# Kernel optimization log

Hardware: AMD Instinct MI355X
Metric: run time of the kernel (lower is better)

## Reference

```python
import jax, jax.numpy as jnp
import numpy as np


def _ln(x, w, b):
    m = x.mean(-1, keepdims=True)
    v = ((x - m) ** 2).mean(-1, keepdims=True)
    return (x - m) / jnp.sqrt(v + 1e-5) * w + b


def setup_inputs() -> dict:
    key = jax.random.key(0)
    ks = jax.random.split(key, 8)
    N, C, H, W = 2, 64, 128, 128
    heads, ksz = 2, 7
    C4 = 4 * C
    p = lambda k, shape: jax.random.normal(k, shape, dtype=jnp.float32) * 0.02
    return {
        "x": jax.random.normal(ks[0], (N, C, H, W), dtype=jnp.float32),
        "qkv_w": p(ks[1], (3 * C, C)),
        "qkv_b": jnp.zeros((3 * C,), jnp.float32),
        "proj_w": p(ks[2], (C, C)),
        "proj_b": jnp.zeros((C,), jnp.float32),
        "rpb": p(ks[3], (heads, 2 * ksz - 1, 2 * ksz - 1)),
        "ln1_w": jnp.ones((C,), jnp.float32),
        "ln1_b": jnp.zeros((C,), jnp.float32),
        "ln2_w": jnp.ones((C,), jnp.float32),
        "ln2_b": jnp.zeros((C,), jnp.float32),
        "fc1_w": p(ks[4], (C4, C)),
        "fc1_b": jnp.zeros((C4,), jnp.float32),
        "fc2_w": p(ks[5], (C, C4)),
        "fc2_b": jnp.zeros((C,), jnp.float32),
    }


def reference(x, qkv_w, qkv_b, proj_w, proj_b, rpb, ln1_w, ln1_b, ln2_w, ln2_b,
              fc1_w, fc1_b, fc2_w, fc2_b):
    N, C, H, W = x.shape
    heads = rpb.shape[0]
    ksz = (rpb.shape[1] + 1) // 2  # kernel size from (2k-1) bias table
    dh = C // heads

    xt = x.transpose(0, 2, 3, 1).reshape(N, H * W, C)  # n (h w) c
    shortcut = xt
    xn = _ln(xt, ln1_w, ln1_b).reshape(N, H, W, C)

    # qkv projection -> (3, N, heads, H, W, dh)
    qkv = (xn @ qkv_w.T + qkv_b).reshape(N, H, W, 3, heads, dh)
    qkv = qkv.transpose(3, 0, 4, 1, 2, 5)
    q = qkv[0] * (dh ** -0.5)
    k = qkv[1]
    v = qkv[2]

    # NATTEN neighborhood: window start clamped so every query sees k x k keys
    sh = jnp.clip(jnp.arange(H) - ksz // 2, 0, H - ksz)
    sw = jnp.clip(jnp.arange(W) - ksz // 2, 0, W - ksz)
    rows = sh[:, None] + jnp.arange(ksz)  # (H, k) key row indices
    cols = sw[:, None] + jnp.arange(ksz)  # (W, k) key col indices

    # relative position bias index: (query - key) + (k-1) in [0, 2k-2]
    rel_h = jnp.arange(H)[:, None] - rows + (ksz - 1)  # (H, k)
    rel_w = jnp.arange(W)[:, None] - cols + (ksz - 1)  # (W, k)
    bias = rpb[:, rel_h][:, :, :, rel_w]               # (heads, H, k, W, k)
    bias = bias.transpose(0, 1, 3, 2, 4)               # (heads, H, W, k, k)

    ri = rows[:, None, :, None]  # (H,1,k,1)
    ci = cols[None, :, None, :]  # (1,W,1,k)
    kwin = k[:, :, ri, ci, :]    # (N, heads, H, W, k, k, dh)
    vwin = v[:, :, ri, ci, :]

    scores = jnp.einsum('nzhwd,nzhwijd->nzhwij', q, kwin) + bias[None]
    attn = jax.nn.softmax(scores.reshape(N, heads, H, W, ksz * ksz), axis=-1)
    out = jnp.einsum('nzhwe,nzhwed->nzhwd', attn,
                     vwin.reshape(N, heads, H, W, ksz * ksz, dh))
    out = out.transpose(0, 2, 3, 1, 4).reshape(N, H, W, C) @ proj_w.T + proj_b

    x2 = shortcut + out.reshape(N, H * W, C)
    y = _ln(x2, ln2_w, ln2_b)
    y = jax.nn.gelu(y @ fc1_w.T + fc1_b, approximate=False) @ fc2_w.T + fc2_b
    x3 = x2 + y
    return x3.reshape(N, H, W, C).transpose(0, 3, 1, 2)
```

## Files before the change

### kernel.cpp

```cpp
#include <hip/hip_runtime.h>
#include <math.h>

#define TQ   32768
#define HWSZ 16384
#define CC   64
#define HH   128
#define WW   128
#define C3   192
#define C4   256
#define KS   7

typedef _Float16 half2v __attribute__((ext_vector_type(2)));
typedef _Float16 half4v __attribute__((ext_vector_type(4)));
typedef _Float16 half8v __attribute__((ext_vector_type(8)));
typedef float    f32x4  __attribute__((ext_vector_type(4)));

#define MFMA16(a, b, c) __builtin_amdgcn_mfma_f32_16x16x32_f16((a), (b), (c), 0, 0, 0)

__global__ __launch_bounds__(256) void k_qkvln(const float* __restrict__ x,
        const float* __restrict__ lnw, const float* __restrict__ lnb,
        const float* __restrict__ qw, const float* __restrict__ qb,
        _Float16* __restrict__ qkv16) {
    __shared__ union {
        struct { __align__(16) _Float16 A[128 * 72]; __align__(16) _Float16 B[192 * 72]; } st;
        __align__(16) _Float16 outb[128 * 200];
    } u;
    __shared__ float ps1[256], ps2[256], m_s[128], r_s[128];
    __shared__ float w_s[64], b_s[64], bias_s[192];
    int tid = threadIdx.x;
    int t0 = blockIdx.x * 128;
    if (tid < 64) { w_s[tid] = lnw[tid]; b_s[tid] = lnb[tid]; }
    if (tid < 192) bias_s[tid] = qb[tid];
    int tok = tid & 127, cq = tid >> 7;
    int t = t0 + tok;
    int n = t >> 14, hw = t & (HWSZ - 1);
    const float* xr = x + ((size_t)n << 20) + hw;
    float v[32];
    float s = 0.f, s2 = 0.f;
#pragma unroll
    for (int e = 0; e < 32; ++e) {
        float f = xr[(cq * 32 + e) * HWSZ];
        v[e] = f; s += f; s2 += f * f;
    }
    ps1[tid] = s; ps2[tid] = s2;
    for (int i = tid; i < 3072; i += 256) {
        int jj = i >> 4, seg = i & 15;
        float4 v4 = *(const float4*)&qw[(size_t)jj * 64 + seg * 4];
        half4v h4 = { (_Float16)v4.x, (_Float16)v4.y, (_Float16)v4.z, (_Float16)v4.w };
        *(half4v*)&u.st.B[jj * 72 + seg * 4] = h4;
    }
    __syncthreads();
    if (tid < 128) {
        float ss = ps1[tid] + ps1[tid + 128];
        float qq = ps2[tid] + ps2[tid + 128];
        float m = ss * (1.f / 64.f);
        float var = qq * (1.f / 64.f) - m * m;
        m_s[tid] = m; r_s[tid] = rsqrtf(var + 1e-5f);
    }
    __syncthreads();
    {
        float m = m_s[tok], r = r_s[tok];
#pragma unroll
        for (int u8 = 0; u8 < 4; ++u8) {
            half8v o;
#pragma unroll
            for (int e = 0; e < 8; ++e) {
                int c = cq * 32 + u8 * 8 + e;
                o[e] = (_Float16)((v[u8 * 8 + e] - m) * r * w_s[c] + b_s[c]);
            }
            *(half8v*)&u.st.A[tok * 72 + cq * 32 + u8 * 8] = o;
        }
    }
    __syncthreads();
    int lane = tid & 63, wv = tid >> 6;
    int quad = lane >> 4, l16 = lane & 15;
    int mt0 = (wv & 1) * 64, nt0 = (wv >> 1) * 96;
    f32x4 acc[4][6];
#pragma unroll
    for (int mf = 0; mf < 4; ++mf)
#pragma unroll
        for (int nf = 0; nf < 6; ++nf) acc[mf][nf] = (f32x4){0.f, 0.f, 0.f, 0.f};
#pragma unroll
    for (int ks = 0; ks < 64; ks += 32) {
        half8v a[4], bfr[6];
#pragma unroll
        for (int mf = 0; mf < 4; ++mf)
            a[mf] = *(const half8v*)&u.st.A[(mt0 + mf * 16 + l16) * 72 + ks + quad * 8];
#pragma unroll
        for (int nf = 0; nf < 6; ++nf)
            bfr[nf] = *(const half8v*)&u.st.B[(nt0 + nf * 16 + l16) * 72 + ks + quad * 8];
#pragma unroll
        for (int mf = 0; mf < 4; ++mf)
#pragma unroll
            for (int nf = 0; nf < 6; ++nf) acc[mf][nf] = MFMA16(a[mf], bfr[nf], acc[mf][nf]);
    }
    __syncthreads();
    const float qscale = 0.17677669529663687f;
#pragma unroll
    for (int mf = 0; mf < 4; ++mf)
#pragma unroll
        for (int nf = 0; nf < 6; ++nf) {
            int j = nt0 + nf * 16 + l16;
            float bias = bias_s[j];
            float sc = (j < 64) ? qscale : 1.f;
#pragma unroll
            for (int r = 0; r < 4; ++r) {
                int tl = mt0 + mf * 16 + quad * 4 + r;
                u.outb[tl * 200 + j] = (_Float16)((acc[mf][nf][r] + bias) * sc);
            }
        }
    __syncthreads();
    for (int i = tid; i < 4096; i += 256) {
        int tk = i >> 5, rem = i & 31;
        if (rem < 24)
            *(half8v*)&qkv16[(size_t)(t0 + tk) * C3 + rem * 8] =
                *(const half8v*)&u.outb[tk * 200 + rem * 8];
    }
}

#define KV_STRIDE 136
#define QS_STRIDE 80
#define SS_STRIDE 50

__global__ __launch_bounds__(256) void k_attn(const _Float16* __restrict__ qkv16,
        const float* __restrict__ rpb, _Float16* __restrict__ out) {
    __shared__ __align__(16) _Float16 kv_s[196 * KV_STRIDE];
    __shared__ __align__(16) _Float16 q_s[64 * QS_STRIDE];
    __shared__ __align__(16) _Float16 s_s[128 * SS_STRIDE];
    __shared__ float rpb_s[338];

    int tid = threadIdx.x;
    int bx = blockIdx.x;
    int n  = bx >> 8;
    int th = (bx >> 4) & 15, tw = bx & 15;
    int h0 = th * 8, w0 = tw * 8;
    int wr0 = min(max(h0 - 3, 0), HH - 14);
    int ww0 = min(max(w0 - 3, 0), WW - 14);
    int tbase = n << 14;

    for (int i = tid; i < 338; i += 256) rpb_s[i] = rpb[i];
    for (int i = tid; i < 196 * 16; i += 256) {
        int tok = i >> 4, u = i & 15;
        int wi = tok / 14, wj = tok - wi * 14;
        *(half8v*)&kv_s[tok * KV_STRIDE + u * 8] = *(const half8v*)&qkv16[
            (size_t)(tbase + (wr0 + wi) * WW + ww0 + wj) * C3 + 64 + u * 8];
    }
    for (int i = tid; i < 64 * 8; i += 256) {
        int q = i >> 3, u = i & 7;
        int qg = tbase + (h0 + (q >> 3)) * WW + (w0 + (q & 7));
        *(half8v*)&q_s[q * QS_STRIDE + u * 8] = *(const half8v*)&qkv16[(size_t)qg * C3 + u * 8];
    }
    __syncthreads();

    int half_ = tid & 1, z = (tid >> 1) & 1, q = tid >> 2;
    int qy = q >> 3, qx = q & 7;
    int h = h0 + qy, wc = w0 + qx;
    int sh = min(max(h - 3, 0), HH - KS);
    int sw = min(max(wc - 3, 0), WW - KS);
    int oh = sh - wr0, ow = sw - ww0;
    int dhp = h - sh + 6, dwp = wc - sw + 6;
    {
        const half8v* qp = (const half8v*)&q_s[q * QS_STRIDE + z * 32];
        half8v q0 = qp[0], q1 = qp[1], q2 = qp[2], q3 = qp[3];
        int i7 = 0, j7 = half_;
        for (int nb = half_; nb < 49; nb += 2) {
            int tok = (oh + i7) * 14 + (ow + j7);
            const half8v* kp = (const half8v*)&kv_s[tok * KV_STRIDE + z * 32];
            half2v acc2 = { (_Float16)0.f, (_Float16)0.f };
            half8v k0 = kp[0], k1 = kp[1], k2 = kp[2], k3 = kp[3];
            acc2 += (half2v){k0.s0, k0.s1} * (half2v){q0.s0, q0.s1};
            acc2 += (half2v){k0.s2, k0.s3} * (half2v){q0.s2, q0.s3};
            acc2 += (half2v){k0.s4, k0.s5} * (half2v){q0.s4, q0.s5};
            acc2 += (half2v){k0.s6, k0.s7} * (half2v){q0.s6, q0.s7};
            acc2 += (half2v){k1.s0, k1.s1} * (half2v){q1.s0, q1.s1};
            acc2 += (half2v){k1.s2, k1.s3} * (half2v){q1.s2, q1.s3};
            acc2 += (half2v){k1.s4, k1.s5} * (half2v){q1.s4, q1.s5};
            acc2 += (half2v){k1.s6, k1.s7} * (half2v){q1.s6, q1.s7};
            acc2 += (half2v){k2.s0, k2.s1} * (half2v){q2.s0, q2.s1};
            acc2 += (half2v){k2.s2, k2.s3} * (half2v){q2.s2, q2.s3};
            acc2 += (half2v){k2.s4, k2.s5} * (half2v){q2.s4, q2.s5};
            acc2 += (half2v){k2.s6, k2.s7} * (half2v){q2.s6, q2.s7};
            acc2 += (half2v){k3.s0, k3.s1} * (half2v){q3.s0, q3.s1};
            acc2 += (half2v){k3.s2, k3.s3} * (half2v){q3.s2, q3.s3};
            acc2 += (half2v){k3.s4, k3.s5} * (half2v){q3.s4, q3.s5};
            acc2 += (half2v){k3.s6, k3.s7} * (half2v){q3.s6, q3.s7};
            float s = (float)acc2.x + (float)acc2.y
                    + rpb_s[(z * 13 + (dhp - i7)) * 13 + (dwp - j7)];
            s_s[(q * 2 + z) * SS_STRIDE + nb] = (_Float16)s;
            j7 += 2;
            if (j7 >= 7) { j7 -= 7; ++i7; }
        }
    }
    __syncthreads();

    if (tid < 128) {
        _Float16* sp = &s_s[tid * SS_STRIDE];
        float mx = -1e30f;
        for (int i = 0; i < 49; ++i) mx = fmaxf(mx, (float)sp[i]);
        float sum = 0.f;
        for (int i = 0; i < 49; ++i) {
            float e = __expf((float)sp[i] - mx);
            sum += e;
            sp[i] = (_Float16)e;
        }
        float inv = 1.f / sum;
        for (int i = 0; i < 49; ++i) sp[i] = (_Float16)((float)sp[i] * inv);
    }
    __syncthreads();

    {
        int c16 = half_;
        const _Float16* pp = &s_s[(q * 2 + z) * SS_STRIDE];
        half2v acc[8];
#pragma unroll
        for (int j = 0; j < 8; ++j) acc[j] = (half2v){ (_Float16)0.f, (_Float16)0.f };
        int i7 = 0, j7 = 0;
        for (int nb = 0; nb < 49; ++nb) {
            int tok = (oh + i7) * 14 + (ow + j7);
            _Float16 p = pp[nb];
            half2v p2 = { p, p };
            const half8v* vp = (const half8v*)&kv_s[tok * KV_STRIDE + 64 + z * 32 + c16 * 16];
            half8v v0 = vp[0], v1 = vp[1];
            acc[0] += (half2v){v0.s0, v0.s1} * p2;
            acc[1] += (half2v){v0.s2, v0.s3} * p2;
            acc[2] += (half2v){v0.s4, v0.s5} * p2;
            acc[3] += (half2v){v0.s6, v0.s7} * p2;
            acc[4] += (half2v){v1.s0, v1.s1} * p2;
            acc[5] += (half2v){v1.s2, v1.s3} * p2;
            acc[6] += (half2v){v1.s4, v1.s5} * p2;
            acc[7] += (half2v){v1.s6, v1.s7} * p2;
            ++j7;
            if (j7 == 7) { j7 = 0; ++i7; }
        }
        int qg = tbase + h * WW + wc;
        _Float16* op = out + (size_t)qg * CC + z * 32 + c16 * 16;
        half8v o0 = {acc[0].x, acc[0].y, acc[1].x, acc[1].y, acc[2].x, acc[2].y, acc[3].x, acc[3].y};
        half8v o1 = {acc[4].x, acc[4].y, acc[5].x, acc[5].y, acc[6].x, acc[6].y, acc[7].x, acc[7].y};
        *(half8v*)op = o0;
        *(half8v*)(op + 8) = o1;
    }
}

__global__ __launch_bounds__(256) void k_projln(const _Float16* __restrict__ ain,
        const float* __restrict__ pw, const float* __restrict__ pb,
        const float* __restrict__ x,
        const float* __restrict__ ln2w, const float* __restrict__ ln2b,
        _Float16* __restrict__ x2_16, _Float16* __restrict__ xn2_16) {
    __shared__ union {
        struct { __align__(16) _Float16 A[128 * 72]; __align__(16) _Float16 B[64 * 72]; } st;
        float x2t[128 * 67];
    } u;
    __shared__ float ps1[256], ps2[256], m_s[128], r_s[128];
    __shared__ float w_s[64], b_s[64], pbias[64];
    int tid = threadIdx.x;
    int t0 = blockIdx.x * 128;
    int n = t0 >> 14, hw0 = t0 & (HWSZ - 1);
    if (tid < 64) { w_s[tid] = ln2w[tid]; b_s[tid] = ln2b[tid]; pbias[tid] = pb[tid]; }
    for (int i = tid; i < 1024; i += 256) {
        int tok = i >> 3, u8 = i & 7;
        *(half8v*)&u.st.A[tok * 72 + u8 * 8] = *(const half8v*)&ain[(size_t)(t0 + tok) * 64 + u8 * 8];
    }
    for (int i = tid; i < 1024; i += 256) {
        int jj = i >> 4, seg = i & 15;
        float4 v4 = *(const float4*)&pw[(size_t)jj * 64 + seg * 4];
        half4v h4 = { (_Float16)v4.x, (_Float16)v4.y, (_Float16)v4.z, (_Float16)v4.w };
        *(half4v*)&u.st.B[jj * 72 + seg * 4] = h4;
    }
    __syncthreads();
    int lane = tid & 63, wv = tid >> 6;
    int quad = lane >> 4, l16 = lane & 15;
    int mt0 = wv * 32;
    f32x4 acc[2][4];
#pragma unroll
    for (int mf = 0; mf < 2; ++mf)
#pragma unroll
        for (int nf = 0; nf < 4; ++nf) acc[mf][nf] = (f32x4){0.f, 0.f, 0.f, 0.f};
#pragma unroll
    for (int ks = 0; ks < 64; ks += 32) {
        half8v a[2], bfr[4];
#pragma unroll
        for (int mf = 0; mf < 2; ++mf)
            a[mf] = *(const half8v*)&u.st.A[(mt0 + mf * 16 + l16) * 72 + ks + quad * 8];
#pragma unroll
        for (int nf = 0; nf < 4; ++nf)
            bfr[nf] = *(const half8v*)&u.st.B[(nf * 16 + l16) * 72 + ks + quad * 8];
#pragma unroll
        for (int mf = 0; mf < 2; ++mf)
#pragma unroll
            for (int nf = 0; nf < 4; ++nf) acc[mf][nf] = MFMA16(a[mf], bfr[nf], acc[mf][nf]);
    }
    __syncthreads();
#pragma unroll
    for (int mf = 0; mf < 2; ++mf)
#pragma unroll
        for (int nf = 0; nf < 4; ++nf) {
            int j = nf * 16 + l16;
            float bias = pbias[j];
            int hwl = hw0 + mt0 + mf * 16 + quad * 4;
            float4 rx = *(const float4*)&x[((size_t)(n * CC + j) << 14) + hwl];
#pragma unroll
            for (int r = 0; r < 4; ++r) {
                int tl = mt0 + mf * 16 + quad * 4 + r;
                u.x2t[tl * 67 + j] = acc[mf][nf][r] + bias + ((const float*)&rx)[r];
            }
        }
    __syncthreads();
    int tok = tid & 127, cq = tid >> 7;
    {
        float s = 0.f, s2 = 0.f;
#pragma unroll
        for (int e = 0; e < 32; ++e) {
            float f = u.x2t[tok * 67 + cq * 32 + e];
            s += f; s2 += f * f;
        }
        ps1[tid] = s; ps2[tid] = s2;
    }
    __syncthreads();
    if (tid < 128) {
        float ss = ps1[tid] + ps1[tid + 128];
        float qq = ps2[tid] + ps2[tid + 128];
        float m = ss * (1.f / 64.f);
        float var = qq * (1.f / 64.f) - m * m;
        m_s[tid] = m; r_s[tid] = rsqrtf(var + 1e-5f);
    }
    __syncthreads();
    {
        float m = m_s[tok], r = r_s[tok];
#pragma unroll
        for (int u8 = 0; u8 < 4; ++u8) {
            half8v hv, nv;
#pragma unroll
            for (int e = 0; e < 8; ++e) {
                int c = cq * 32 + u8 * 8 + e;
                float f = u.x2t[tok * 67 + c];
                hv[e] = (_Float16)f;
                nv[e] = (_Float16)((f - m) * r * w_s[c] + b_s[c]);
            }
            size_t base = (size_t)(t0 + tok) * 64 + cq * 32 + u8 * 8;
            *(half8v*)&x2_16[base] = hv;
            *(half8v*)&xn2_16[base] = nv;
        }
    }
}

__global__ __launch_bounds__(256) void k_fc1(const _Float16* __restrict__ xin,
        const float* __restrict__ fw, const float* __restrict__ fb,
        _Float16* __restrict__ hbuf16) {
    __shared__ __align__(16) _Float16 A_s[128 * 72];
    __shared__ __align__(16) _Float16 B_s[128 * 72];
    __shared__ float bias_s[128];
    int tid = threadIdx.x;
    int t0 = (blockIdx.x >> 1) * 128;
    int j0 = (blockIdx.x & 1) * 128;
    for (int i = tid; i < 1024; i += 256) {
        int tok = i >> 3, u8 = i & 7;
        *(half8v*)&A_s[tok * 72 + u8 * 8] = *(const half8v*)&xin[(size_t)(t0 + tok) * 64 + u8 * 8];
    }
    for (int i = tid; i < 2048; i += 256) {
        int jj = i >> 4, seg = i & 15;
        float4 v4 = *(const float4*)&fw[(size_t)(j0 + jj) * 64 + seg * 4];
        half4v h4 = { (_Float16)v4.x, (_Float16)v4.y, (_Float16)v4.z, (_Float16)v4.w };
        *(half4v*)&B_s[jj * 72 + seg * 4] = h4;
    }
    if (tid < 128) bias_s[tid] = fb[j0 + tid];
    __syncthreads();
    int lane = tid & 63, wv = tid >> 6;
    int quad = lane >> 4, l16 = lane & 15;
    int mt0 = (wv & 1) * 64, nt0 = (wv >> 1) * 64;
    f32x4 acc[4][4];
#pragma unroll
    for (int mf = 0; mf < 4; ++mf)
#pragma unroll
        for (int nf = 0; nf < 4; ++nf) acc[mf][nf] = (f32x4){0.f, 0.f, 0.f, 0.f};
#pragma unroll
    for (int ks = 0; ks < 64; ks += 32) {
        half8v a[4], bfr[4];
#pragma unroll
        for (int mf = 0; mf < 4; ++mf)
            a[mf] = *(const half8v*)&A_s[(mt0 + mf * 16 + l16) * 72 + ks + quad * 8];
#pragma unroll
        for (int nf = 0; nf < 4; ++nf)
            bfr[nf] = *(const half8v*)&B_s[(nt0 + nf * 16 + l16) * 72 + ks + quad * 8];
#pragma unroll
        for (int mf = 0; mf < 4; ++mf)
#pragma unroll
            for (int nf = 0; nf < 4; ++nf) acc[mf][nf] = MFMA16(a[mf], bfr[nf], acc[mf][nf]);
    }
#pragma unroll
    for (int mf = 0; mf < 4; ++mf)
#pragma unroll
        for (int nf = 0; nf < 4; ++nf) {
            int j = j0 + nt0 + nf * 16 + l16;
            float bias = bias_s[nt0 + nf * 16 + l16];
#pragma unroll
            for (int r = 0; r < 4; ++r) {
                int t = t0 + mt0 + mf * 16 + quad * 4 + r;
                float v = acc[mf][nf][r] + bias;
                float g = 0.5f * v * (1.f + erff(v * 0.70710678118654752f));
                hbuf16[(size_t)t * C4 + j] = (_Float16)g;
            }
        }
}

__global__ __launch_bounds__(256) void k_fc2(const _Float16* __restrict__ hbuf16,
        const float* __restrict__ fw, const float* __restrict__ fb,
        const _Float16* __restrict__ x2_16, float* __restrict__ out) {
    __shared__ union {
        struct { __align__(16) _Float16 A[128 * 72]; __align__(16) _Float16 B[64 * 72]; } st;
        float tr[64 * 132];
    } u;
    __shared__ float fb_s[64];
    int tid = threadIdx.x;
    int t0 = blockIdx.x * 128;
    int lane = tid & 63, wv = tid >> 6;
    int quad = lane >> 4, l16 = lane & 15;
    int mt0 = wv * 32;
    if (tid < 64) fb_s[tid] = fb[tid];
    f32x4 acc[2][4];
#pragma unroll
    for (int mf = 0; mf < 2; ++mf)
#pragma unroll
        for (int nf = 0; nf < 4; ++nf) acc[mf][nf] = (f32x4){0.f, 0.f, 0.f, 0.f};
    for (int kp = 0; kp < 4; ++kp) {
        if (kp) __syncthreads();
        for (int i = tid; i < 1024; i += 256) {
            int tok = i >> 3, u8 = i & 7;
            *(half8v*)&u.st.A[tok * 72 + u8 * 8] =
                *(const half8v*)&hbuf16[(size_t)(t0 + tok) * C4 + kp * 64 + u8 * 8];
        }
        for (int i = tid; i < 1024; i += 256) {
            int jj = i >> 4, seg = i & 15;
            float4 v4 = *(const float4*)&fw[(size_t)jj * C4 + kp * 64 + seg * 4];
            half4v h4 = { (_Float16)v4.x, (_Float16)v4.y, (_Float16)v4.z, (_Float16)v4.w };
            *(half4v*)&u.st.B[jj * 72 + seg * 4] = h4;
        }
        __syncthreads();
#pragma unroll
        for (int ks = 0; ks < 64; ks += 32) {
            half8v a[2], bfr[4];
#pragma unroll
            for (int mf = 0; mf < 2; ++mf)
                a[mf] = *(const half8v*)&u.st.A[(mt0 + mf * 16 + l16) * 72 + ks + quad * 8];
#pragma unroll
            for (int nf = 0; nf < 4; ++nf)
                bfr[nf] = *(const half8v*)&u.st.B[(nf * 16 + l16) * 72 + ks + quad * 8];
#pragma unroll
            for (int mf = 0; mf < 2; ++mf)
#pragma unroll
                for (int nf = 0; nf < 4; ++nf) acc[mf][nf] = MFMA16(a[mf], bfr[nf], acc[mf][nf]);
        }
    }
    __syncthreads();
#pragma unroll
    for (int mf = 0; mf < 2; ++mf)
#pragma unroll
        for (int nf = 0; nf < 4; ++nf) {
            int j = nf * 16 + l16;
            float bias = fb_s[j];
#pragma unroll
            for (int r = 0; r < 4; ++r) {
                int tl = mt0 + mf * 16 + quad * 4 + r;
                float v = acc[mf][nf][r] + bias + (float)x2_16[(size_t)(t0 + tl) * 64 + j];
                u.tr[j * 132 + tl] = v;
            }
        }
    __syncthreads();
    int n = t0 >> 14, hw0 = t0 & (HWSZ - 1);
    for (int i = tid; i < 64 * 32; i += 256) {
        int j = i >> 5, seg = i & 31;
        float4 v = *(const float4*)&u.tr[j * 132 + seg * 4];
        *(float4*)&out[((size_t)(n * CC + j) << 14) + hw0 + seg * 4] = v;
    }
}

extern "C" void kernel_launch(void* const* d_in, const int* in_sizes, int n_in,
                              void* d_out, int out_size, void* d_ws, size_t ws_size,
                              hipStream_t stream) {
    const float* x      = (const float*)d_in[0];
    const float* qkv_w  = (const float*)d_in[1];
    const float* qkv_b  = (const float*)d_in[2];
    const float* proj_w = (const float*)d_in[3];
    const float* proj_b = (const float*)d_in[4];
    const float* rpb    = (const float*)d_in[5];
    const float* ln1_w  = (const float*)d_in[6];
    const float* ln1_b  = (const float*)d_in[7];
    const float* ln2_w  = (const float*)d_in[8];
    const float* ln2_b  = (const float*)d_in[9];
    const float* fc1_w  = (const float*)d_in[10];
    const float* fc1_b  = (const float*)d_in[11];
    const float* fc2_w  = (const float*)d_in[12];
    const float* fc2_b  = (const float*)d_in[13];
    float* out = (float*)d_out;
    char* ws = (char*)d_ws;

    _Float16* qkv16  = (_Float16*)(ws);
    _Float16* attn16 = (_Float16*)(ws + 12582912);
    _Float16* x2_16  = (_Float16*)(ws + 16777216);
    _Float16* xn2_16 = (_Float16*)(ws + 20971520);
    _Float16* hbuf16 = (_Float16*)(ws + 25165824);

    k_qkvln <<<256, 256, 0, stream>>>(x, ln1_w, ln1_b, qkv_w, qkv_b, qkv16);
    k_attn  <<<512, 256, 0, stream>>>(qkv16, rpb, attn16);
    k_projln<<<256, 256, 0, stream>>>(attn16, proj_w, proj_b, x, ln2_w, ln2_b, x2_16, xn2_16);
    k_fc1   <<<512, 256, 0, stream>>>(xn2_16, fc1_w, fc1_b, hbuf16);
    k_fc2   <<<256, 256, 0, stream>>>(hbuf16, fc2_w, fc2_b, x2_16, out);
}
```

Baseline: 149.6 us.

## Fuse fc1 and fc2 into one MLP kernel keeping hidden activations in LDS

```diff
diff --git a/kernel.cpp b/kernel.cpp
--- a/kernel.cpp
+++ b/kernel.cpp
@@ -343,132 +343,113 @@
     }
 }
 
-__global__ __launch_bounds__(256) void k_fc1(const _Float16* __restrict__ xin,
-        const float* __restrict__ fw, const float* __restrict__ fb,
-        _Float16* __restrict__ hbuf16) {
-    __shared__ __align__(16) _Float16 A_s[128 * 72];
-    __shared__ __align__(16) _Float16 B_s[128 * 72];
-    __shared__ float bias_s[128];
+__global__ __launch_bounds__(256) void k_mlp(const _Float16* __restrict__ xn2,
+        const _Float16* __restrict__ x2_16,
+        const float* __restrict__ f1w, const float* __restrict__ f1b,
+        const float* __restrict__ f2w, const float* __restrict__ f2b,
+        float* __restrict__ out) {
+    __shared__ __align__(16) _Float16 H_s[64 * 264];
+    __shared__ union {
+        struct { __align__(16) _Float16 A[64 * 72]; __align__(16) _Float16 B[128 * 72]; } st;
+        float tr[64 * 68];
+    } u;
+    __shared__ float f1b_s[256], f2b_s[64];
     int tid = threadIdx.x;
-    int t0 = (blockIdx.x >> 1) * 128;
-    int j0 = (blockIdx.x & 1) * 128;
-    for (int i = tid; i < 1024; i += 256) {
-        int tok = i >> 3, u8 = i & 7;
-        *(half8v*)&A_s[tok * 72 + u8 * 8] = *(const half8v*)&xin[(size_t)(t0 + tok) * 64 + u8 * 8];
-    }
-    for (int i = tid; i < 2048; i += 256) {
-        int jj = i >> 4, seg = i & 15;
-        float4 v4 = *(const float4*)&fw[(size_t)(j0 + jj) * 64 + seg * 4];
-        half4v h4 = { (_Float16)v4.x, (_Float16)v4.y, (_Float16)v4.z, (_Float16)v4.w };
-        *(half4v*)&B_s[jj * 72 + seg * 4] = h4;
-    }
-    if (tid < 128) bias_s[tid] = fb[j0 + tid];
-    __syncthreads();
+    int t0 = blockIdx.x * 64;
     int lane = tid & 63, wv = tid >> 6;
     int quad = lane >> 4, l16 = lane & 15;
-    int mt0 = (wv & 1) * 64, nt0 = (wv >> 1) * 64;
-    f32x4 acc[4][4];
-#pragma unroll
-    for (int mf = 0; mf < 4; ++mf)
-#pragma unroll
-        for (int nf = 0; nf < 4; ++nf) acc[mf][nf] = (f32x4){0.f, 0.f, 0.f, 0.f};
-#pragma unroll
-    for (int ks = 0; ks < 64; ks += 32) {
-        half8v a[4], bfr[4];
-#pragma unroll
-        for (int mf = 0; mf < 4; ++mf)
-            a[mf] = *(const half8v*)&A_s[(mt0 + mf * 16 + l16) * 72 + ks + quad * 8];
-#pragma unroll
-        for (int nf = 0; nf < 4; ++nf)
-            bfr[nf] = *(const half8v*)&B_s[(nt0 + nf * 16 + l16) * 72 + ks + quad * 8];
-#pragma unroll
-        for (int mf = 0; mf < 4; ++mf)
-#pragma unroll
-            for (int nf = 0; nf < 4; ++nf) acc[mf][nf] = MFMA16(a[mf], bfr[nf], acc[mf][nf]);
-    }
-#pragma unroll
-    for (int mf = 0; mf < 4; ++mf)
-#pragma unroll
-        for (int nf = 0; nf < 4; ++nf) {
-            int j = j0 + nt0 + nf * 16 + l16;
-            float bias = bias_s[nt0 + nf * 16 + l16];
-#pragma unroll
-            for (int r = 0; r < 4; ++r) {
-                int t = t0 + mt0 + mf * 16 + quad * 4 + r;
-                float v = acc[mf][nf][r] + bias;
-                float g = 0.5f * v * (1.f + erff(v * 0.70710678118654752f));
-                hbuf16[(size_t)t * C4 + j] = (_Float16)g;
+    f1b_s[tid] = f1b[tid];
+    if (tid < 64) f2b_s[tid] = f2b[tid];
+    for (int i = tid; i < 512; i += 256) {
+        int tok = i >> 3, u8 = i & 7;
+        *(half8v*)&u.st.A[tok * 72 + u8 * 8] = *(const half8v*)&xn2[(size_t)(t0 + tok) * 64 + u8 * 8];
+    }
+    for (int jh = 0; jh < 2; ++jh) {
+        if (jh) __syncthreads();
+        for (int i = tid; i < 2048; i += 256) {
+            int jj = i >> 4, seg = i & 15;
+            float4 v4 = *(const float4*)&f1w[(size_t)(jh * 128 + jj) * 64 + seg * 4];
+            half4v h4 = { (_Float16)v4.x, (_Float16)v4.y, (_Float16)v4.z, (_Float16)v4.w };
+            *(half4v*)&u.st.B[jj * 72 + seg * 4] = h4;
+        }
+        __syncthreads();
+        int mt0 = (wv & 1) * 32, nt0 = (wv >> 1) * 64;
+        f32x4 acc[2][4];
+#pragma unroll
+        for (int mf = 0; mf < 2; ++mf)
+#pragma unroll
+            for (int nf = 0; nf < 4; ++nf) acc[mf][nf] = (f32x4){0.f, 0.f, 0.f, 0.f};
+#pragma unroll
+        for (int ks = 0; ks < 64; ks += 32) {
+            half8v a[2], bfr[4];
+#pragma unroll
+            for (int mf = 0; mf < 2; ++mf)
+                a[mf] = *(const half8v*)&u.st.A[(mt0 + mf * 16 + l16) * 72 + ks + quad * 8];
+#pragma unroll
+            for (int nf = 0; nf < 4; ++nf)
+                bfr[nf] = *(const half8v*)&u.st.B[(nt0 + nf * 16 + l16) * 72 + ks + quad * 8];
+#pragma unroll
+            for (int mf = 0; mf < 2; ++mf)
+#pragma unroll
+                for (int nf = 0; nf < 4; ++nf) acc[mf][nf] = MFMA16(a[mf], bfr[nf], acc[mf][nf]);
+        }
+#pragma unroll
+        for (int mf = 0; mf < 2; ++mf)
+#pragma unroll
+            for (int nf = 0; nf < 4; ++nf) {
+                int jl = nt0 + nf * 16 + l16;
+                float bias = f1b_s[jh * 128 + jl];
+#pragma unroll
+                for (int r = 0; r < 4; ++r) {
+                    int tl = mt0 + mf * 16 + quad * 4 + r;
+                    float vv = acc[mf][nf][r] + bias;
+                    float g = 0.5f * vv * (1.f + erff(vv * 0.70710678118654752f));
+                    H_s[tl * 264 + jh * 128 + jl] = (_Float16)g;
+                }
             }
-        }
-}
-
-__global__ __launch_bounds__(256) void k_fc2(const _Float16* __restrict__ hbuf16,
-        const float* __restrict__ fw, const float* __restrict__ fb,
-        const _Float16* __restrict__ x2_16, float* __restrict__ out) {
-    __shared__ union {
-        struct { __align__(16) _Float16 A[128 * 72]; __align__(16) _Float16 B[64 * 72]; } st;
-        float tr[64 * 132];
-    } u;
-    __shared__ float fb_s[64];
-    int tid = threadIdx.x;
-    int t0 = blockIdx.x * 128;
-    int lane = tid & 63, wv = tid >> 6;
-    int quad = lane >> 4, l16 = lane & 15;
-    int mt0 = wv * 32;
-    if (tid < 64) fb_s[tid] = fb[tid];
-    f32x4 acc[2][4];
-#pragma unroll
-    for (int mf = 0; mf < 2; ++mf)
-#pragma unroll
-        for (int nf = 0; nf < 4; ++nf) acc[mf][nf] = (f32x4){0.f, 0.f, 0.f, 0.f};
+    }
+    __syncthreads();
+    int mt0 = wv * 16;
+    f32x4 acc2[4];
+#pragma unroll
+    for (int nf = 0; nf < 4; ++nf) acc2[nf] = (f32x4){0.f, 0.f, 0.f, 0.f};
     for (int kp = 0; kp < 4; ++kp) {
         if (kp) __syncthreads();
         for (int i = tid; i < 1024; i += 256) {
-            int tok = i >> 3, u8 = i & 7;
-            *(half8v*)&u.st.A[tok * 72 + u8 * 8] =
-                *(const half8v*)&hbuf16[(size_t)(t0 + tok) * C4 + kp * 64 + u8 * 8];
-        }
-        for (int i = tid; i < 1024; i += 256) {
             int jj = i >> 4, seg = i & 15;
-            float4 v4 = *(const float4*)&fw[(size_t)jj * C4 + kp * 64 + seg * 4];
+            float4 v4 = *(const float4*)&f2w[(size_t)jj * C4 + kp * 64 + seg * 4];
             half4v h4 = { (_Float16)v4.x, (_Float16)v4.y, (_Float16)v4.z, (_Float16)v4.w };
             *(half4v*)&u.st.B[jj * 72 + seg * 4] = h4;
         }
         __syncthreads();
 #pragma unroll
         for (int ks = 0; ks < 64; ks += 32) {
-            half8v a[2], bfr[4];
-#pragma unroll
-            for (int mf = 0; mf < 2; ++mf)
-                a[mf] = *(const half8v*)&u.st.A[(mt0 + mf * 16 + l16) * 72 + ks + quad * 8];
+            half8v a = *(const half8v*)&H_s[(mt0 + l16) * 264 + kp * 64 + ks + quad * 8];
+            half8v bfr[4];
 #pragma unroll
             for (int nf = 0; nf < 4; ++nf)
                 bfr[nf] = *(const half8v*)&u.st.B[(nf * 16 + l16) * 72 + ks + quad * 8];
 #pragma unroll
-            for (int mf = 0; mf < 2; ++mf)
-#pragma unroll
-                for (int nf = 0; nf < 4; ++nf) acc[mf][nf] = MFMA16(a[mf], bfr[nf], acc[mf][nf]);
-        }
-    }
-    __syncthreads();
-#pragma unroll
-    for (int mf = 0; mf < 2; ++mf)
-#pragma unroll
-        for (int nf = 0; nf < 4; ++nf) {
-            int j = nf * 16 + l16;
-            float bias = fb_s[j];
-#pragma unroll
-            for (int r = 0; r < 4; ++r) {
-                int tl = mt0 + mf * 16 + quad * 4 + r;
-                float v = acc[mf][nf][r] + bias + (float)x2_16[(size_t)(t0 + tl) * 64 + j];
-                u.tr[j * 132 + tl] = v;
-            }
-        }
+            for (int nf = 0; nf < 4; ++nf) acc2[nf] = MFMA16(a, bfr[nf], acc2[nf]);
+        }
+    }
+    __syncthreads();
+#pragma unroll
+    for (int nf = 0; nf < 4; ++nf) {
+        int j = nf * 16 + l16;
+        float bias = f2b_s[j];
+#pragma unroll
+        for (int r = 0; r < 4; ++r) {
+            int tl = mt0 + quad * 4 + r;
+            float v = acc2[nf][r] + bias + (float)x2_16[(size_t)(t0 + tl) * 64 + j];
+            u.tr[j * 68 + tl] = v;
+        }
+    }
     __syncthreads();
     int n = t0 >> 14, hw0 = t0 & (HWSZ - 1);
-    for (int i = tid; i < 64 * 32; i += 256) {
-        int j = i >> 5, seg = i & 31;
-        float4 v = *(const float4*)&u.tr[j * 132 + seg * 4];
+    for (int i = tid; i < 1024; i += 256) {
+        int j = i >> 4, seg = i & 15;
+        float4 v = *(const float4*)&u.tr[j * 68 + seg * 4];
         *(float4*)&out[((size_t)(n * CC + j) << 14) + hw0 + seg * 4] = v;
     }
 }
@@ -497,11 +478,9 @@
     _Float16* attn16 = (_Float16*)(ws + 12582912);
     _Float16* x2_16  = (_Float16*)(ws + 16777216);
     _Float16* xn2_16 = (_Float16*)(ws + 20971520);
-    _Float16* hbuf16 = (_Float16*)(ws + 25165824);
 
     k_qkvln <<<256, 256, 0, stream>>>(x, ln1_w, ln1_b, qkv_w, qkv_b, qkv16);
     k_attn  <<<512, 256, 0, stream>>>(qkv16, rpb, attn16);
     k_projln<<<256, 256, 0, stream>>>(attn16, proj_w, proj_b, x, ln2_w, ln2_b, x2_16, xn2_16);
-    k_fc1   <<<512, 256, 0, stream>>>(xn2_16, fc1_w, fc1_b, hbuf16);
-    k_fc2   <<<256, 256, 0, stream>>>(hbuf16, fc2_w, fc2_b, x2_16, out);
+    k_mlp   <<<512, 256, 0, stream>>>(xn2_16, x2_16, fc1_w, fc1_b, fc2_w, fc2_b, out);
 }
```

Result: faster. 142.9 us (-4.5%).
